# Kernel tuning notes

Hardware: AMD Instinct MI355X
Metric: run time of the kernel (lower is better)

## Reference

```python
import jax, jax.numpy as jnp
import numpy as np

N = 100000   # nodes
E = 1600000  # edges (avg degree 16)
IN, HID, CLS = 256, 128, 64

def setup_inputs() -> dict:
    key = jax.random.key(0)
    ks = jax.random.split(key, 7)
    x = jax.random.normal(ks[0], (N, IN), dtype=jnp.float32)
    src = jax.random.randint(ks[1], (E,), 0, N, dtype=jnp.int32)
    dst = jax.random.randint(ks[2], (E,), 0, N, dtype=jnp.int32)
    # glorot-ish init for GraphConv weights
    W1 = jax.random.normal(ks[3], (IN, HID), dtype=jnp.float32) * (1.0 / np.sqrt(IN))
    W2 = jax.random.normal(ks[4], (HID, HID), dtype=jnp.float32) * (1.0 / np.sqrt(HID))
    W3 = jax.random.normal(ks[5], (HID, CLS), dtype=jnp.float32) * (1.0 / np.sqrt(HID))
    b1 = jnp.zeros((HID,), jnp.float32)
    b2 = jnp.zeros((HID,), jnp.float32)
    b3 = jnp.zeros((CLS,), jnp.float32)
    return {"x": x, "src": src, "dst": dst, "W1": W1, "b1": b1,
            "W2": W2, "b2": b2, "W3": W3, "b3": b3}


def _graph_conv(h, src, dst, W, b, out_norm, in_norm):
    """DGL GraphConv with norm='both', allow_zero_in_degree=True."""
    in_f, out_f = W.shape
    h = h * out_norm[:, None]                 # src-side degree norm
    if in_f > out_f:
        # transform first (fewer flops), then aggregate
        h = h @ W
        agg = jax.ops.segment_sum(h[src], dst, num_segments=N)
    else:
        agg = jax.ops.segment_sum(h[src], dst, num_segments=N)
        agg = agg @ W
    return agg * in_norm[:, None] + b         # dst-side norm + bias


def reference(x, src, dst, W1, b1, W2, b2, W3, b3):
    ones = jnp.ones((E,), jnp.float32)
    out_deg = jax.ops.segment_sum(ones, src, num_segments=N)
    in_deg = jax.ops.segment_sum(ones, dst, num_segments=N)
    out_norm = jnp.clip(out_deg, 1.0) ** -0.5
    in_norm = jnp.clip(in_deg, 1.0) ** -0.5

    h = _graph_conv(x, src, dst, W1, b1, out_norm, in_norm)
    h = jax.nn.relu(h)  # dropout = identity in eval mode
    h = _graph_conv(h, src, dst, W2, b2, out_norm, in_norm)
    h = jax.nn.relu(h)
    h = _graph_conv(h, src, dst, W3, b3, out_norm, in_norm)
    return h
```

## Files before the change

kernel.cpp:

```cpp
#include <hip/hip_runtime.h>

#define NN 100000
#define NE 1600000
#define FIN 256
#define FHID 128
#define FCLS 64

#define SH1 9
#define P1 196
#define EPB_H 2048
#define NBH ((NE + EPB_H - 1) / EPB_H)
#define EPB_P 4096
#define NBP ((NE + EPB_P - 1) / EPB_P)
#define BROWS 4

typedef _Float16 f16;
typedef __attribute__((ext_vector_type(8))) _Float16 f16x8;
typedef __attribute__((ext_vector_type(2))) _Float16 f16x2;
typedef __attribute__((ext_vector_type(4))) float f32x4;
typedef __attribute__((ext_vector_type(2))) float f32x2;

__global__ __launch_bounds__(256) void k_histA(const int* __restrict__ src, const int* __restrict__ dst,
                                               int* __restrict__ hist2d, int* __restrict__ shist2d) {
  __shared__ int lh[P1], lhS[P1];
  int t = threadIdx.x;
  for (int i = t; i < P1; i += 256) { lh[i] = 0; lhS[i] = 0; }
  __syncthreads();
  int base = blockIdx.x * EPB_H;
  int cnt = NE - base; if (cnt > EPB_H) cnt = EPB_H;
  for (int i = t; i < cnt; i += 256) {
    atomicAdd(&lh[dst[base + i] >> SH1], 1);
    atomicAdd(&lhS[src[base + i] >> SH1], 1);
  }
  __syncthreads();
  for (int i = t; i < P1; i += 256) {
    hist2d[blockIdx.x * P1 + i] = lh[i];
    shist2d[blockIdx.x * P1 + i] = lhS[i];
  }
}

__global__ __launch_bounds__(256) void k_colscan2(const int* __restrict__ hist2d, const int* __restrict__ shist2d,
                                                  int* __restrict__ colpre, int* __restrict__ colpreS,
                                                  int* __restrict__ totals, int* __restrict__ totalsS) {
  __shared__ int sm[256];
  int bp = blockIdx.x;
  bool isS = bp >= P1;
  int p = isS ? bp - P1 : bp;
  const int* h = isS ? shist2d : hist2d;
  int* cp = isS ? colpreS : colpre;
  int* tt = isS ? totalsS : totals;
  int t = threadIdx.x;
  int vals[BROWS];
  int lsum = 0;
  int b0 = t * BROWS;
#pragma unroll
  for (int i = 0; i < BROWS; ++i) {
    int b = b0 + i;
    int v = (b < NBH) ? h[b * P1 + p] : 0;
    vals[i] = v;
    lsum += v;
  }
  int x = lsum;
  sm[t] = x;
  __syncthreads();
  for (int off = 1; off < 256; off <<= 1) {
    int y = (t >= off) ? sm[t - off] : 0;
    __syncthreads();
    x += y;
    sm[t] = x;
    __syncthreads();
  }
  int run = x - lsum;
#pragma unroll
  for (int i = 0; i < BROWS; ++i) {
    int b = b0 + i;
    if (b < NBH) cp[b * P1 + p] = run;
    run += vals[i];
  }
  if (t == 255) tt[p] = x;
}

__global__ __launch_bounds__(256) void k_pbase2(const int* __restrict__ totals, const int* __restrict__ totalsS,
                                                int* __restrict__ pbase, int* __restrict__ pbaseS,
                                                int* __restrict__ rp) {
  __shared__ int sm[256];
  int t = threadIdx.x;
  int v = (t < P1) ? totals[t] : 0;
  int x = v;
  sm[t] = x;
  __syncthreads();
  for (int off = 1; off < 256; off <<= 1) {
    int y = (t >= off) ? sm[t - off] : 0;
    __syncthreads();
    x += y;
    sm[t] = x;
    __syncthreads();
  }
  if (t < P1) pbase[t] = x - v;
  __syncthreads();
  int vS = (t < P1) ? totalsS[t] : 0;
  int xS = vS;
  sm[t] = xS;
  __syncthreads();
  for (int off = 1; off < 256; off <<= 1) {
    int y = (t >= off) ? sm[t - off] : 0;
    __syncthreads();
    xS += y;
    sm[t] = xS;
    __syncthreads();
  }
  if (t < P1) pbaseS[t] = xS - vS;
  if (t == 0) rp[NN] = NE;
}

__global__ __launch_bounds__(256) void k_place(const int* __restrict__ src, const int* __restrict__ dst,
                                               const int* __restrict__ hist2d, const int* __restrict__ shist2d,
                                               const int* __restrict__ colpre, const int* __restrict__ colpreS,
                                               const int* __restrict__ pbase, const int* __restrict__ pbaseS,
                                               unsigned* __restrict__ staged, unsigned short* __restrict__ stagedS) {
  __shared__ unsigned buf[EPB_P];
  __shared__ unsigned bufS[EPB_P];
  __shared__ unsigned char prt[EPB_P];
  __shared__ int lofs[P1], lcur[P1], lbase[P1];
  __shared__ int lofsS[P1], lcurS[P1], lbaseS[P1];
  __shared__ int sm[256];
  int t = threadIdx.x;
  int b = blockIdx.x;
  int f0 = 2 * b, f1 = 2 * b + 1;
  int v = 0, vS = 0;
  if (t < P1) {
    v = hist2d[f0 * P1 + t];
    vS = shist2d[f0 * P1 + t];
    if (f1 < NBH) { v += hist2d[f1 * P1 + t]; vS += shist2d[f1 * P1 + t]; }
    lbase[t] = pbase[t] + colpre[f0 * P1 + t];
    lbaseS[t] = pbaseS[t] + colpreS[f0 * P1 + t];
    lcur[t] = 0;
    lcurS[t] = 0;
  }
  int x = v;
  sm[t] = x;
  __syncthreads();
  for (int off = 1; off < 256; off <<= 1) {
    int y = (t >= off) ? sm[t - off] : 0;
    __syncthreads();
    x += y;
    sm[t] = x;
    __syncthreads();
  }
  if (t < P1) lofs[t] = x - v;
  __syncthreads();
  int xS = vS;
  sm[t] = xS;
  __syncthreads();
  for (int off = 1; off < 256; off <<= 1) {
    int y = (t >= off) ? sm[t - off] : 0;
    __syncthreads();
    xS += y;
    sm[t] = xS;
    __syncthreads();
  }
  if (t < P1) lofsS[t] = xS - vS;
  __syncthreads();

  int base = b * EPB_P;
  int cnt = NE - base; if (cnt > EPB_P) cnt = EPB_P;
  for (int i = t; i < cnt; i += 256) {
    int s = src[base + i], d = dst[base + i];
    int p = d >> SH1;
    int pos = lofs[p] + atomicAdd(&lcur[p], 1);
    buf[pos] = ((unsigned)s << SH1) | (unsigned)(d & 511);
    prt[pos] = (unsigned char)p;
    int pS = s >> SH1;
    int posS = lofsS[pS] + atomicAdd(&lcurS[pS], 1);
    bufS[posS] = (unsigned)s;
  }
  __syncthreads();
  for (int i = t; i < cnt; i += 256) {
    int p = prt[i];
    staged[lbase[p] + (i - lofs[p])] = buf[i];
    unsigned sv = bufS[i];
    int pS = sv >> SH1;
    stagedS[lbaseS[pS] + (i - lofsS[pS])] = (unsigned short)(sv & 511);
  }
}

__global__ __launch_bounds__(512) void k_buildp(const unsigned* __restrict__ staged, const int* __restrict__ totals,
                                                const int* __restrict__ pbase, int* __restrict__ rp,
                                                float* __restrict__ inorm, int* __restrict__ csr) {
  __shared__ int lcnt[512], lofs[512], lcur[512];
  int p = blockIdx.x, t = threadIdx.x;
  int pb = pbase[p], cnt = totals[p];
  lcnt[t] = 0;
  __syncthreads();
  const unsigned* sp = staged + pb;
  for (int i = t; i < cnt; i += 512) atomicAdd(&lcnt[sp[i] & 511], 1);
  __syncthreads();
  int v = lcnt[t];
  int x = v;
  lofs[t] = x;
  __syncthreads();
  for (int off = 1; off < 512; off <<= 1) {
    int y = (t >= off) ? lofs[t - off] : 0;
    __syncthreads();
    x += y;
    lofs[t] = x;
    __syncthreads();
  }
  int excl = x - v;
  lofs[t] = excl;
  lcur[t] = 0;
  int node = (p << SH1) + t;
  if (node < NN) {
    rp[node] = pb + excl;
    int dg = v < 1 ? 1 : v;
    inorm[node] = rsqrtf((float)dg);
  }
  __syncthreads();
  for (int i = t; i < cnt; i += 512) {
    unsigned e = sp[i];
    int d = e & 511;
    int pos = pb + lofs[d] + atomicAdd(&lcur[d], 1);
    csr[pos] = (int)(e >> SH1);
  }
}

__global__ __launch_bounds__(512) void k_countS(const unsigned short* __restrict__ stagedS,
                                                const int* __restrict__ totalsS, const int* __restrict__ pbaseS,
                                                float* __restrict__ onorm) {
  __shared__ int lcnt[512];
  int p = blockIdx.x, t = threadIdx.x;
  int pb = pbaseS[p], cnt = totalsS[p];
  lcnt[t] = 0;
  __syncthreads();
  const unsigned short* sp = stagedS + pb;
  for (int i = t; i < cnt; i += 512) atomicAdd(&lcnt[sp[i]], 1);
  __syncthreads();
  int node = (p << SH1) + t;
  if (node < NN) {
    int od = lcnt[t];
    if (od < 1) od = 1;
    onorm[node] = rsqrtf((float)od);
  }
}

template <int K, int NW>
__global__ __launch_bounds__(256) void k_packw(const float* __restrict__ W, f16* __restrict__ Wp) {
  int idx = blockIdx.x * 256 + threadIdx.x;
  if (idx >= K * NW) return;
  constexpr int nT = NW / 16;
  int i = idx & 7;
  int l = (idx >> 3) & 63;
  int rest = idx >> 9;
  int t = rest % nT;
  int s = rest / nT;
  int k = s * 32 + (l >> 4) * 8 + i;
  int n = t * 16 + (l & 15);
  Wp[idx] = (f16)W[k * NW + n];
}

template <int K, int NW, int MODE>
__global__ __launch_bounds__(256) void k_gemm(const void* __restrict__ Asrc, const f16* __restrict__ Wp,
                                              const float* __restrict__ onorm, const float* __restrict__ bias,
                                              f16* __restrict__ Out) {
  constexpr int nS = K / 32, nT = NW / 16;
  int lane = threadIdx.x & 63;
  int w = threadIdx.x >> 6;
  int bm = blockIdx.x * 64 + w * 16;
  int arow = bm + (lane & 15);
  int koff = (lane >> 4) * 8;
  bool rowok = arow < NN;

  f32x4 acc[nT];
#pragma unroll
  for (int t = 0; t < nT; ++t) acc[t] = (f32x4){0.f, 0.f, 0.f, 0.f};

  float ascale = 0.0f;
  if (MODE == 0) ascale = rowok ? onorm[arow] : 0.0f;

  for (int s = 0; s < nS; ++s) {
    f16x8 a = {};
    if (rowok) {
      if (MODE == 0) {
        const float* ap = (const float*)Asrc + (size_t)arow * K + s * 32 + koff;
        f32x4 v0 = *(const f32x4*)ap;
        f32x4 v1 = *(const f32x4*)(ap + 4);
#pragma unroll
        for (int j = 0; j < 4; ++j) {
          a[j] = (f16)(v0[j] * ascale);
          a[4 + j] = (f16)(v1[j] * ascale);
        }
      } else {
        a = *(const f16x8*)((const f16*)Asrc + ((size_t)s * NN + arow) * 32 + koff);
      }
    }
    const f16* bp = Wp + ((size_t)(s * nT) * 64 + lane) * 8;
#pragma unroll
    for (int t = 0; t < nT; ++t) {
      f16x8 bfr = *(const f16x8*)(bp + t * 512);
      acc[t] = __builtin_amdgcn_mfma_f32_16x16x32_f16(a, bfr, acc[t], 0, 0, 0);
    }
  }

  int crow0 = bm + (lane >> 4) * 4;
  int ccol = lane & 15;
#pragma unroll
  for (int t = 0; t < nT; ++t) {
#pragma unroll
    for (int r = 0; r < 4; ++r) {
      int row = crow0 + r;
      if (row >= NN) continue;
      int col = t * 16 + ccol;
      float v = acc[t][r];
      if (MODE == 2) v = fmaxf(v + bias[col], 0.f) * onorm[row];
      Out[((size_t)(col >> 5) * NN + row) * 32 + (col & 31)] = (f16)v;
    }
  }
}

#define LCSR_CAP 1408
template <int NS, int MODE>
__global__ __launch_bounds__(256) void k_aggs(const f16* __restrict__ src_arr, const int* __restrict__ rp,
                                              const int* __restrict__ csr, const float* __restrict__ inorm,
                                              const float* __restrict__ onorm, const float* __restrict__ bias,
                                              void* __restrict__ outp) {
  constexpr int XPS = 8 / NS;
  constexpr int BPS = (NN + 63) / 64;
  __shared__ int lcsr[LCSR_CAP];
  int bid = blockIdx.x;
  int r = bid & 7;
  int slice = r / XPS;
  int w = (bid >> 3) * XPS + (r % XPS);
  if (w >= BPS) return;
  int t = threadIdx.x;
  int nbase = w * 64;
  int nlim = nbase + 64; if (nlim > NN) nlim = NN;
  int first = rp[nbase];
  int last = rp[nlim];
  int span = last - first;
  bool useLds = (span <= LCSR_CAP);
  if (useLds) {
    for (int i = t; i < span; i += 256) lcsr[i] = csr[first + i];
  }
  __syncthreads();
  int node = nbase + (t >> 2);
  if (node >= NN) return;
  int q = t & 3;
  int beg = rp[node], end = rp[node + 1];
  const char* sbp = (const char*)src_arr + ((size_t)slice * NN * 32 + q * 8) * 2;

  float acc[8];
#pragma unroll
  for (int j = 0; j < 8; ++j) acc[j] = 0.f;

  if (useLds) {
    int le = beg - first, lend = end - first;
    for (; le + 7 < lend; le += 8) {
      int x0 = lcsr[le], x1 = lcsr[le + 1], x2 = lcsr[le + 2], x3 = lcsr[le + 3];
      int x4 = lcsr[le + 4], x5 = lcsr[le + 5], x6 = lcsr[le + 6], x7 = lcsr[le + 7];
      f16x8 v0 = *(const f16x8*)(sbp + ((size_t)(unsigned)x0 << 6));
      f16x8 v1 = *(const f16x8*)(sbp + ((size_t)(unsigned)x1 << 6));
      f16x8 v2 = *(const f16x8*)(sbp + ((size_t)(unsigned)x2 << 6));
      f16x8 v3 = *(const f16x8*)(sbp + ((size_t)(unsigned)x3 << 6));
      f16x8 v4 = *(const f16x8*)(sbp + ((size_t)(unsigned)x4 << 6));
      f16x8 v5 = *(const f16x8*)(sbp + ((size_t)(unsigned)x5 << 6));
      f16x8 v6 = *(const f16x8*)(sbp + ((size_t)(unsigned)x6 << 6));
      f16x8 v7 = *(const f16x8*)(sbp + ((size_t)(unsigned)x7 << 6));
#pragma unroll
      for (int j = 0; j < 8; ++j) {
        float s01 = (float)v0[j] + (float)v1[j];
        float s23 = (float)v2[j] + (float)v3[j];
        float s45 = (float)v4[j] + (float)v5[j];
        float s67 = (float)v6[j] + (float)v7[j];
        acc[j] += (s01 + s23) + (s45 + s67);
      }
    }
    for (; le + 3 < lend; le += 4) {
      int x0 = lcsr[le], x1 = lcsr[le + 1], x2 = lcsr[le + 2], x3 = lcsr[le + 3];
      f16x8 v0 = *(const f16x8*)(sbp + ((size_t)(unsigned)x0 << 6));
      f16x8 v1 = *(const f16x8*)(sbp + ((size_t)(unsigned)x1 << 6));
      f16x8 v2 = *(const f16x8*)(sbp + ((size_t)(unsigned)x2 << 6));
      f16x8 v3 = *(const f16x8*)(sbp + ((size_t)(unsigned)x3 << 6));
#pragma unroll
      for (int j = 0; j < 8; ++j)
        acc[j] += ((float)v0[j] + (float)v1[j]) + ((float)v2[j] + (float)v3[j]);
    }
    for (; le < lend; ++le) {
      f16x8 v0 = *(const f16x8*)(sbp + ((size_t)(unsigned)lcsr[le] << 6));
#pragma unroll
      for (int j = 0; j < 8; ++j) acc[j] += (float)v0[j];
    }
  } else {
    for (int e = beg; e < end; ++e) {
      f16x8 v0 = *(const f16x8*)(sbp + ((size_t)(unsigned)csr[e] << 6));
#pragma unroll
      for (int j = 0; j < 8; ++j) acc[j] += (float)v0[j];
    }
  }

  float inn = inorm[node];
  int gfb = slice * 32 + q * 8;
  if (MODE == 0) {
    float on = onorm[node];
    f16x8 o;
#pragma unroll
    for (int j = 0; j < 8; ++j) o[j] = (f16)(fmaxf(acc[j] * inn + bias[gfb + j], 0.f) * on);
    *(f16x8*)((f16*)outp + ((size_t)slice * NN + node) * 32 + q * 8) = o;
  } else if (MODE == 1) {
    f16x8 o;
#pragma unroll
    for (int j = 0; j < 8; ++j) o[j] = (f16)(acc[j] * inn);
    *(f16x8*)((f16*)outp + ((size_t)slice * NN + node) * 32 + q * 8) = o;
  } else {
    float* op = (float*)outp + (size_t)node * (NS * 32) + gfb;
    f32x4 o0, o1;
#pragma unroll
    for (int j = 0; j < 4; ++j) {
      o0[j] = acc[j] * inn + bias[gfb + j];
      o1[j] = acc[4 + j] * inn + bias[gfb + 4 + j];
    }
    *(f32x4*)op = o0;
    *(f32x4*)(op + 4) = o1;
  }
}

extern "C" void kernel_launch(void* const* d_in, const int* in_sizes, int n_in,
                              void* d_out, int out_size, void* d_ws, size_t ws_size,
                              hipStream_t stream) {
  const float* x = (const float*)d_in[0];
  const int* src = (const int*)d_in[1];
  const int* dst = (const int*)d_in[2];
  const float* W1 = (const float*)d_in[3];
  const float* b1 = (const float*)d_in[4];
  const float* W2 = (const float*)d_in[5];
  const float* b2 = (const float*)d_in[6];
  const float* W3 = (const float*)d_in[7];
  const float* b3 = (const float*)d_in[8];

  char* base = (char*)d_ws;
  size_t off = 0;
  auto take = [&](size_t bytes) -> void* {
    void* r = base + off;
    off += (bytes + 255) & ~(size_t)255;
    return r;
  };
  float* onorm = (float*)take((size_t)NN * 4);
  float* inorm = (float*)take((size_t)NN * 4);
  int* rp = (int*)take((size_t)(NN + 1) * 4);
  int* totals = (int*)take((size_t)P1 * 4);
  int* totalsS = (int*)take((size_t)P1 * 4);
  int* pbase = (int*)take((size_t)P1 * 4);
  int* pbaseS = (int*)take((size_t)P1 * 4);
  int* hist2d = (int*)take((size_t)NBH * P1 * 4);
  int* shist2d = (int*)take((size_t)NBH * P1 * 4);
  int* colpre = (int*)take((size_t)NBH * P1 * 4);
  int* colpreS = (int*)take((size_t)NBH * P1 * 4);
  unsigned* staged = (unsigned*)take((size_t)NE * 4);
  unsigned short* stagedS = (unsigned short*)take((size_t)NE * 2);
  int* csr = (int*)take((size_t)NE * 4);
  f16* W1p = (f16*)take((size_t)FIN * FHID * 2);
  f16* W2p = (f16*)take((size_t)FHID * FHID * 2);
  f16* W3p = (f16*)take((size_t)FHID * FCLS * 2);
  f16* B1 = (f16*)take((size_t)NN * FHID * 2);
  f16* B2 = (f16*)take((size_t)NN * FHID * 2);

  k_histA<<<NBH, 256, 0, stream>>>(src, dst, hist2d, shist2d);
  k_colscan2<<<2 * P1, 256, 0, stream>>>(hist2d, shist2d, colpre, colpreS, totals, totalsS);
  k_pbase2<<<1, 256, 0, stream>>>(totals, totalsS, pbase, pbaseS, rp);
  k_place<<<NBP, 256, 0, stream>>>(src, dst, hist2d, shist2d, colpre, colpreS, pbase, pbaseS, staged, stagedS);
  k_buildp<<<P1, 512, 0, stream>>>(staged, totals, pbase, rp, inorm, csr);
  k_countS<<<P1, 512, 0, stream>>>(stagedS, totalsS, pbaseS, onorm);

  k_packw<FIN, FHID><<<(FIN * FHID + 255) / 256, 256, 0, stream>>>(W1, W1p);
  k_packw<FHID, FHID><<<(FHID * FHID + 255) / 256, 256, 0, stream>>>(W2, W2p);
  k_packw<FHID, FCLS><<<(FHID * FCLS + 255) / 256, 256, 0, stream>>>(W3, W3p);

  const int gemm_grid = (NN + 63) / 64;
  const int bps = (NN + 63) / 64;
  const int agg4_grid = ((bps + 1) / 2) * 8;
  const int agg2_grid = ((bps + 3) / 4) * 8;
  k_gemm<FIN, FHID, 0><<<gemm_grid, 256, 0, stream>>>(x, W1p, onorm, nullptr, B1);
  k_aggs<4, 0><<<agg4_grid, 256, 0, stream>>>(B1, rp, csr, inorm, onorm, b1, B2);
  k_aggs<4, 1><<<agg4_grid, 256, 0, stream>>>(B2, rp, csr, inorm, nullptr, nullptr, B1);
  k_gemm<FHID, FHID, 2><<<gemm_grid, 256, 0, stream>>>(B1, W2p, onorm, b2, B2);
  k_gemm<FHID, FCLS, 1><<<gemm_grid, 256, 0, stream>>>(B2, W3p, nullptr, nullptr, B1);
  k_aggs<2, 2><<<agg2_grid, 256, 0, stream>>>(B1, rp, csr, inorm, nullptr, b3, d_out);
}
```

Measured before the change: 286.2 us.

## Pre-cast scaled input to sliced f16 layout and prefetch A fragments in GEMM

Adds a kernel that scales x by the out-degree norm and converts it to f16 in the sliced layout, so the first GEMM can use the f16 path. The f16 GEMM path now preloads a window of A fragments ahead of the MFMA loop to hide load latency. This adds an extra pass over x and extra workspace, used only if the workspace is large enough.

```diff
diff --git a/kernel.cpp b/kernel.cpp
--- a/kernel.cpp
+++ b/kernel.cpp
@@ -243,6 +243,27 @@
   }
 }
 
+__global__ __launch_bounds__(256) void k_cast(const float* __restrict__ x, const float* __restrict__ onorm,
+                                              f16* __restrict__ xh) {
+  int g = blockIdx.x * 256 + threadIdx.x;
+  if (g >= NN * 32) return;
+  int node = g >> 5;
+  int ko = (g & 31) * 8;
+  int slice = ko >> 5;
+  int j = ko & 31;
+  float on = onorm[node];
+  const float* xp = x + (size_t)node * FIN + ko;
+  f32x4 v0 = *(const f32x4*)xp;
+  f32x4 v1 = *(const f32x4*)(xp + 4);
+  f16x8 o;
+#pragma unroll
+  for (int i = 0; i < 4; ++i) {
+    o[i] = (f16)(v0[i] * on);
+    o[4 + i] = (f16)(v1[i] * on);
+  }
+  *(f16x8*)(xh + ((size_t)slice * NN + node) * 32 + j) = o;
+}
+
 template <int K, int NW>
 __global__ __launch_bounds__(256) void k_packw(const float* __restrict__ W, f16* __restrict__ Wp) {
   int idx = blockIdx.x * 256 + threadIdx.x;
@@ -274,13 +295,11 @@
 #pragma unroll
   for (int t = 0; t < nT; ++t) acc[t] = (f32x4){0.f, 0.f, 0.f, 0.f};
 
-  float ascale = 0.0f;
-  if (MODE == 0) ascale = rowok ? onorm[arow] : 0.0f;
-
-  for (int s = 0; s < nS; ++s) {
-    f16x8 a = {};
-    if (rowok) {
-      if (MODE == 0) {
+  if (MODE == 0) {
+    float ascale = rowok ? onorm[arow] : 0.0f;
+    for (int s = 0; s < nS; ++s) {
+      f16x8 a = {};
+      if (rowok) {
         const float* ap = (const float*)Asrc + (size_t)arow * K + s * 32 + koff;
         f32x4 v0 = *(const f32x4*)ap;
         f32x4 v1 = *(const f32x4*)(ap + 4);
@@ -289,15 +308,31 @@
           a[j] = (f16)(v0[j] * ascale);
           a[4 + j] = (f16)(v1[j] * ascale);
         }
-      } else {
-        a = *(const f16x8*)((const f16*)Asrc + ((size_t)s * NN + arow) * 32 + koff);
       }
-    }
-    const f16* bp = Wp + ((size_t)(s * nT) * 64 + lane) * 8;
-#pragma unroll
-    for (int t = 0; t < nT; ++t) {
-      f16x8 bfr = *(const f16x8*)(bp + t * 512);
-      acc[t] = __builtin_amdgcn_mfma_f32_16x16x32_f16(a, bfr, acc[t], 0, 0, 0);
+      const f16* bp = Wp + ((size_t)(s * nT) * 64 + lane) * 8;
+#pragma unroll
+      for (int t = 0; t < nT; ++t) {
+        f16x8 bfr = *(const f16x8*)(bp + t * 512);
+        acc[t] = __builtin_amdgcn_mfma_f32_16x16x32_f16(a, bfr, acc[t], 0, 0, 0);
+      }
+    }
+  } else {
+    constexpr int WIN = nS < 4 ? nS : 4;
+    const f16* abase = (const f16*)Asrc + (size_t)arow * 32 + koff;
+    f16x8 af[nS];
+#pragma unroll
+    for (int s = 0; s < WIN; ++s)
+      af[s] = rowok ? *(const f16x8*)(abase + (size_t)s * NN * 32) : (f16x8){};
+#pragma unroll
+    for (int s = 0; s < nS; ++s) {
+      if (s + WIN < nS)
+        af[s + WIN] = rowok ? *(const f16x8*)(abase + (size_t)(s + WIN) * NN * 32) : (f16x8){};
+      const f16* bp = Wp + ((size_t)(s * nT) * 64 + lane) * 8;
+#pragma unroll
+      for (int t = 0; t < nT; ++t) {
+        f16x8 bfr = *(const f16x8*)(bp + t * 512);
+        acc[t] = __builtin_amdgcn_mfma_f32_16x16x32_f16(af[s], bfr, acc[t], 0, 0, 0);
+      }
     }
   }
 
@@ -462,6 +497,9 @@
   f16* W3p = (f16*)take((size_t)FHID * FCLS * 2);
   f16* B1 = (f16*)take((size_t)NN * FHID * 2);
   f16* B2 = (f16*)take((size_t)NN * FHID * 2);
+  size_t xh_bytes = (size_t)NN * FIN * 2;
+  bool useCast = (off + xh_bytes + 256 <= ws_size);
+  f16* xh = useCast ? (f16*)take(xh_bytes) : nullptr;
 
   k_histA<<<NBH, 256, 0, stream>>>(src, dst, hist2d, shist2d);
   k_colscan2<<<2 * P1, 256, 0, stream>>>(hist2d, shist2d, colpre, colpreS, totals, totalsS);
@@ -478,7 +516,13 @@
   const int bps = (NN + 63) / 64;
   const int agg4_grid = ((bps + 1) / 2) * 8;
   const int agg2_grid = ((bps + 3) / 4) * 8;
-  k_gemm<FIN, FHID, 0><<<gemm_grid, 256, 0, stream>>>(x, W1p, onorm, nullptr, B1);
+
+  if (useCast) {
+    k_cast<<<(NN * 32 + 255) / 256, 256, 0, stream>>>(x, onorm, xh);
+    k_gemm<FIN, FHID, 1><<<gemm_grid, 256, 0, stream>>>(xh, W1p, nullptr, nullptr, B1);
+  } else {
+    k_gemm<FIN, FHID, 0><<<gemm_grid, 256, 0, stream>>>(x, W1p, onorm, nullptr, B1);
+  }
   k_aggs<4, 0><<<agg4_grid, 256, 0, stream>>>(B1, rp, csr, inorm, onorm, b1, B2);
   k_aggs<4, 1><<<agg4_grid, 256, 0, stream>>>(B2, rp, csr, inorm, nullptr, nullptr, B1);
   k_gemm<FHID, FHID, 2><<<gemm_grid, 256, 0, stream>>>(B1, W2p, onorm, b2, B2);
```

Result: slower. 297.7 us (+4.0%).
